# Kernel optimization log

Measured on AMD Instinct MI355X. Metric: run time of the kernel, lower is better.

Reference implementation:

```python
import jax, jax.numpy as jnp
import numpy as np

RADIUS = 8
STRIDE = 4
EPS = 1e-5
B, N, C, O = 4, 16384, 64, 64
S = 2 * RADIUS


def _bn(x, gamma, beta, mean, var):
    # inference-mode BatchNorm1d
    return (x - mean) / jnp.sqrt(var + EPS) * gamma + beta


def _circular_grouping_index(batch, n_points):
    # neighbors at circular offsets -radius..-1, 1..radius along the point sequence
    offsets = jnp.concatenate([jnp.arange(-RADIUS, 0), jnp.arange(1, RADIUS + 1)])  # (S,)
    idx = (jnp.arange(n_points)[:, None] + offsets[None, :]) % n_points             # (N,S)
    gidx = jnp.arange(batch)[:, None, None] * n_points + idx[None]                  # (B,N,S)
    return gidx.reshape(-1)


def setup_inputs() -> dict:
    key = jax.random.key(0)
    ks = jax.random.split(key, 8)
    inp = {
        "points": jax.random.normal(ks[0], (B, N, 2), dtype=jnp.float32),
        "features": jax.random.normal(ks[1], (B * N, C), dtype=jnp.float32),
        # modules_1: Linear(2+C -> C, no bias), BN(C), ReLU, Linear(C -> 1)
        "w1": jax.random.normal(ks[2], (2 + C, C), dtype=jnp.float32) * 0.05,
        "bn1_gamma": jnp.ones((C,), jnp.float32),
        "bn1_beta": jnp.zeros((C,), jnp.float32),
        "bn1_mean": jnp.zeros((C,), jnp.float32),
        "bn1_var": jnp.ones((C,), jnp.float32),
        "w2": jax.random.normal(ks[3], (C, 1), dtype=jnp.float32) * 0.05,
        "b2": jnp.zeros((1,), jnp.float32),
        # modules_2: Linear(C -> O, no bias), BN(O), ReLU
        "w3": jax.random.normal(ks[4], (C, O), dtype=jnp.float32) * 0.05,
        "bn2_gamma": jnp.ones((O,), jnp.float32),
        "bn2_beta": jnp.zeros((O,), jnp.float32),
        "bn2_mean": jnp.zeros((O,), jnp.float32),
        "bn2_var": jnp.ones((O,), jnp.float32),
    }
    return inp


def reference(points, features, w1, bn1_gamma, bn1_beta, bn1_mean, bn1_var,
              w2, b2, w3, bn2_gamma, bn2_beta, bn2_mean, bn2_var):
    batch, n_points, _ = points.shape
    gidx = _circular_grouping_index(batch, n_points)                 # (B*N*S,)

    nn_points = points.reshape(-1, 2)[gidx].reshape(batch, n_points, S, 2)
    translation = (nn_points - points[:, :, None])[:, ::STRIDE].reshape(-1, 2)

    nn_features = features[gidx].reshape(batch, n_points, S, -1)     # (B,N,S,C)
    nn_feat_str = nn_features[:, ::STRIDE].reshape(-1, features.shape[1])

    # attention weights
    h = jnp.concatenate([translation, nn_feat_str], axis=1) @ w1
    h = jax.nn.relu(_bn(h, bn1_gamma, bn1_beta, bn1_mean, bn1_var))
    w = h @ w2 + b2                                                  # (-1,1)
    w = jax.nn.softmax(w.reshape(-1, S, 1), axis=1)

    # value branch (computed on all gathered rows, then strided, as in original)
    y = jax.nn.relu(_bn(features[gidx] @ w3, bn2_gamma, bn2_beta, bn2_mean, bn2_var))
    y = y.reshape(batch, n_points, S, -1)[:, ::STRIDE].reshape(-1, S, O)

    outputs = jnp.sum(y * w, axis=1)                                 # (B*N/stride, O)
    points_out = points[:, ::STRIDE]
    return points_out, outputs
```

## Files before the change

kernel.cpp:

```cpp
#include <hip/hip_runtime.h>
#include <hip/hip_bf16.h>

#define NPTS   16384
#define NMASK  16383
#define EPSV   1e-5f
#define OUTOFF 32768

typedef __attribute__((ext_vector_type(8))) short short8_t;
typedef __attribute__((ext_vector_type(4))) short short4_t;
typedef __attribute__((ext_vector_type(4))) float f32x4;

static __device__ __forceinline__ short f2bf(float x) {
    union { __hip_bfloat16 b; short s; } u; u.b = __float2bfloat16(x); return u.s;
}
static __device__ __forceinline__ float bf2f(short s) {
    union { float f; unsigned u; } v; v.u = ((unsigned)(unsigned short)s) << 16; return v.f;
}

__global__ __launch_bounds__(512, 2) void fused_std_kernel(
    const float* __restrict__ points,
    const float* __restrict__ features,
    const float* __restrict__ w1,
    const float* __restrict__ bn1_gamma, const float* __restrict__ bn1_beta,
    const float* __restrict__ bn1_mean,  const float* __restrict__ bn1_var,
    const float* __restrict__ w2,
    const float* __restrict__ w3,
    const float* __restrict__ bn2_gamma, const float* __restrict__ bn2_beta,
    const float* __restrict__ bn2_mean,  const float* __restrict__ bn2_var,
    float* __restrict__ d_out)
{
    __shared__ __align__(16) short glds[288 * 64];
    __shared__ __align__(16) short ylds[288 * 64];
    __shared__ __align__(16) float ptsl[288 * 2];
    __shared__ __align__(16) float cst[448];
    __shared__ __align__(16) float ebuf[64][16];

    const float* cP  = cst;
    const float* cQ  = cst + 64;
    const float* cW2 = cst + 128;
    const float* cS1 = cst + 192;
    const float* cB1 = cst + 256;
    const float* cS2 = cst + 320;
    const float* cB2 = cst + 384;

    const int tid = threadIdx.x;
    const int wv  = tid >> 6, l = tid & 63;
    const int r   = l & 15,  kg = l >> 4;
    const int bi  = blockIdx.x >> 6;
    const int n0  = (blockIdx.x & 63) * 256;
    const int base = bi * NPTS;

    struct TF { float4 a, b, c, d; };
    auto loadTile = [&](int ti) {
        const int gr = base + ((n0 - 16 + ti * 16 + r) & NMASK);
        const float* fp = features + (size_t)gr * 64 + kg * 8;
        TF t;
        t.a = *(const float4*)(fp);
        t.b = *(const float4*)(fp + 4);
        t.c = *(const float4*)(fp + 32);
        t.d = *(const float4*)(fp + 36);
        return t;
    };
    TF Ta = loadTile(wv);
    TF Tb = loadTile(wv + 8);
    TF Tc;
    if (wv < 2) Tc = loadTile(16 + wv);

    short8_t wf[2][4][2];
    #pragma unroll
    for (int mat = 0; mat < 2; ++mat) {
        const float* wsrc = mat ? w3 : (w1 + 128);
        #pragma unroll
        for (int tt = 0; tt < 4; ++tt)
            #pragma unroll
            for (int s = 0; s < 2; ++s) {
                const float* p0 = wsrc + (s * 32 + kg * 8) * 64 + 16 * tt + r;
                short8_t w;
                #pragma unroll
                for (int e = 0; e < 8; ++e) w[e] = f2bf(p0[e * 64]);
                wf[mat][tt][s] = w;
            }
    }

    if (tid < 64) {
        const float s1 = bn1_gamma[tid] * rsqrtf(bn1_var[tid] + EPSV);
        cst[tid]       = s1 * w1[tid];
        cst[64 + tid]  = s1 * w1[64 + tid];
        cst[128 + tid] = w2[tid];
        cst[192 + tid] = s1;
        cst[256 + tid] = bn1_beta[tid] - bn1_mean[tid] * s1;
        const float s2 = bn2_gamma[tid] * rsqrtf(bn2_var[tid] + EPSV);
        cst[320 + tid] = s2;
        cst[384 + tid] = bn2_beta[tid] - bn2_mean[tid] * s2;
    }
    for (int t = tid; t < 288; t += 512) {
        const int gr = base + ((n0 - 16 + t) & NMASK);
        *(float2*)&ptsl[t * 2] = *(const float2*)&points[(size_t)gr * 2];
    }
    __syncthreads();

    auto mfma_tile = [&](const TF& t, int ti) {
        short8_t f0, f1;
        f0[0]=f2bf(t.a.x); f0[1]=f2bf(t.a.y); f0[2]=f2bf(t.a.z); f0[3]=f2bf(t.a.w);
        f0[4]=f2bf(t.b.x); f0[5]=f2bf(t.b.y); f0[6]=f2bf(t.b.z); f0[7]=f2bf(t.b.w);
        f1[0]=f2bf(t.c.x); f1[1]=f2bf(t.c.y); f1[2]=f2bf(t.c.z); f1[3]=f2bf(t.c.w);
        f1[4]=f2bf(t.d.x); f1[5]=f2bf(t.d.y); f1[6]=f2bf(t.d.z); f1[7]=f2bf(t.d.w);
        const f32x4 z = {0.f, 0.f, 0.f, 0.f};
        f32x4 acc0[4] = {z, z, z, z}, acc1[4] = {z, z, z, z};
        #pragma unroll
        for (int tt = 0; tt < 4; ++tt) {
            #pragma unroll
            for (int s = 0; s < 2; ++s) {
                acc0[tt] = __builtin_amdgcn_mfma_f32_16x16x32_bf16(wf[0][tt][s], s ? f1 : f0, acc0[tt], 0, 0, 0);
                acc1[tt] = __builtin_amdgcn_mfma_f32_16x16x32_bf16(wf[1][tt][s], s ? f1 : f0, acc1[tt], 0, 0, 0);
            }
        }
        const int row = ti * 16 + r;
        #pragma unroll
        for (int tt = 0; tt < 4; ++tt) {
            const int c0 = 16 * tt + kg * 4;
            short4_t gq, yq;
            #pragma unroll
            for (int j = 0; j < 4; ++j) {
                gq[j] = f2bf(fmaf(acc0[tt][j], cS1[c0 + j], cB1[c0 + j]));
                yq[j] = f2bf(fmaxf(fmaf(acc1[tt][j], cS2[c0 + j], cB2[c0 + j]), 0.0f));
            }
            const int byte = row * 128 +
                (((2 * tt + (kg >> 1)) ^ (row & 7)) << 4) + ((kg & 1) << 3);
            *(short4_t*)((char*)glds + byte) = gq;
            *(short4_t*)((char*)ylds + byte) = yq;
        }
    };
    mfma_tile(Ta, wv);
    mfma_tile(Tb, wv + 8);
    if (wv < 2) mfma_tile(Tc, 16 + wv);
    __syncthreads();

    const int offk = (r < 8) ? r - 8 : r - 7;
    const f32x4 P0a = *(const f32x4*)&cP[kg * 8],      P0b = *(const f32x4*)&cP[kg * 8 + 4];
    const f32x4 P1a = *(const f32x4*)&cP[32 + kg * 8], P1b = *(const f32x4*)&cP[32 + kg * 8 + 4];
    const f32x4 Q0a = *(const f32x4*)&cQ[kg * 8],      Q0b = *(const f32x4*)&cQ[kg * 8 + 4];
    const f32x4 Q1a = *(const f32x4*)&cQ[32 + kg * 8], Q1b = *(const f32x4*)&cQ[32 + kg * 8 + 4];
    const f32x4 Wa  = *(const f32x4*)&cW2[kg * 8],     Wb  = *(const f32x4*)&cW2[kg * 8 + 4];
    const f32x4 Wc  = *(const f32x4*)&cW2[32 + kg * 8],Wd  = *(const f32x4*)&cW2[32 + kg * 8 + 4];

    #pragma unroll 1
    for (int i = 0; i < 8; ++i) {
        const int p = wv * 8 + i;
        const int crow = 16 + 4 * p;
        const int nrow = crow + offk;
        const float2 cpt = *(const float2*)&ptsl[crow * 2];
        const float2 npt = *(const float2*)&ptsl[nrow * 2];
        const float tx = npt.x - cpt.x, ty = npt.y - cpt.y;
        const short8_t g0 = *(const short8_t*)((const char*)glds +
            nrow * 128 + ((kg ^ (nrow & 7)) << 4));
        const short8_t g1 = *(const short8_t*)((const char*)glds +
            nrow * 128 + (((4 + kg) ^ (nrow & 7)) << 4));
        float s = 0.0f;
        #pragma unroll
        for (int e = 0; e < 4; ++e) {
            s = fmaf(fmaxf(bf2f(g0[e])     + tx * P0a[e] + ty * Q0a[e], 0.f), Wa[e], s);
            s = fmaf(fmaxf(bf2f(g0[e + 4]) + tx * P0b[e] + ty * Q0b[e], 0.f), Wb[e], s);
            s = fmaf(fmaxf(bf2f(g1[e])     + tx * P1a[e] + ty * Q1a[e], 0.f), Wc[e], s);
            s = fmaf(fmaxf(bf2f(g1[e + 4]) + tx * P1b[e] + ty * Q1b[e], 0.f), Wd[e], s);
        }
        s += __shfl_xor(s, 16);
        s += __shfl_xor(s, 32);

        float mx = s;
        mx = fmaxf(mx, __shfl_xor(mx, 1));
        mx = fmaxf(mx, __shfl_xor(mx, 2));
        mx = fmaxf(mx, __shfl_xor(mx, 4));
        mx = fmaxf(mx, __shfl_xor(mx, 8));
        const float ex = __expf(s - mx);
        float se = ex;
        se += __shfl_xor(se, 1);
        se += __shfl_xor(se, 2);
        se += __shfl_xor(se, 4);
        se += __shfl_xor(se, 8);
        if (l < 16) ebuf[p][l] = ex / se;
    }
    asm volatile("s_waitcnt lgkmcnt(0)" ::: "memory");

    #pragma unroll 1
    for (int i = 0; i < 8; ++i) {
        const int p = wv * 8 + i;
        const int crow = 16 + 4 * p;
        const f32x4 wA = *(const f32x4*)&ebuf[p][0];
        const f32x4 wB = *(const f32x4*)&ebuf[p][4];
        const f32x4 wC = *(const f32x4*)&ebuf[p][8];
        const f32x4 wD = *(const f32x4*)&ebuf[p][12];
        float o = 0.0f;
        #pragma unroll
        for (int k = 0; k < 16; ++k) {
            const float wk = (k < 4) ? wA[k] : (k < 8) ? wB[k - 4]
                            : (k < 12) ? wC[k - 8] : wD[k - 12];
            const int rk = crow + ((k < 8) ? k - 8 : k - 7);
            const short yb = *(const short*)((const char*)ylds +
                rk * 128 + (((l >> 3) ^ (rk & 7)) << 4) + ((l & 7) << 1));
            o = fmaf(wk, bf2f(yb), o);
        }
        const int pl = ((blockIdx.x & 63) << 6) + p;
        d_out[OUTOFF + ((size_t)bi * 4096 + pl) * 64 + l] = o;
        if (l < 2)
            d_out[((size_t)bi * 4096 + pl) * 2 + l] = ptsl[crow * 2 + l];
    }
}

extern "C" void kernel_launch(void* const* d_in, const int* in_sizes, int n_in,
                              void* d_out, int out_size, void* d_ws, size_t ws_size,
                              hipStream_t stream)
{
    const float* points    = (const float*)d_in[0];
    const float* features  = (const float*)d_in[1];
    const float* w1        = (const float*)d_in[2];
    const float* bn1_gamma = (const float*)d_in[3];
    const float* bn1_beta  = (const float*)d_in[4];
    const float* bn1_mean  = (const float*)d_in[5];
    const float* bn1_var   = (const float*)d_in[6];
    const float* w2        = (const float*)d_in[7];
    const float* w3        = (const float*)d_in[9];
    const float* bn2_gamma = (const float*)d_in[10];
    const float* bn2_beta  = (const float*)d_in[11];
    const float* bn2_mean  = (const float*)d_in[12];
    const float* bn2_var   = (const float*)d_in[13];

    fused_std_kernel<<<256, 512, 0, stream>>>(
        points, features, w1, bn1_gamma, bn1_beta, bn1_mean, bn1_var,
        w2, w3, bn2_gamma, bn2_beta, bn2_mean, bn2_var, (float*)d_out);
}
```

Baseline: 20.75 us.

## Give each wave a private halo slice to drop the block-wide barrier

Each wave now computes the MFMA projections for its own 48-row window, which includes its halo, and stores them in a per-wave LDS slice. This replaces the shared 288-row buffer and the __syncthreads between the projection and attention phases with a per-wave lgkmcnt wait. In exchange, halo rows are recomputed, so every wave now does three tiles instead of two or three (48 rows per wave against 288 shared rows). LDS use also grows from 288 to 384 rows per buffer, which could limit occupancy.

```diff
diff --git a/kernel.cpp b/kernel.cpp
--- a/kernel.cpp
+++ b/kernel.cpp
@@ -29,8 +29,8 @@
     const float* __restrict__ bn2_mean,  const float* __restrict__ bn2_var,
     float* __restrict__ d_out)
 {
-    __shared__ __align__(16) short glds[288 * 64];
-    __shared__ __align__(16) short ylds[288 * 64];
+    __shared__ __align__(16) short glds[8][48 * 64];
+    __shared__ __align__(16) short ylds[8][48 * 64];
     __shared__ __align__(16) float ptsl[288 * 2];
     __shared__ __align__(16) float cst[448];
     __shared__ __align__(16) float ebuf[64][16];
@@ -49,10 +49,11 @@
     const int bi  = blockIdx.x >> 6;
     const int n0  = (blockIdx.x & 63) * 256;
     const int base = bi * NPTS;
+    const int Lw  = 32 * wv + 8;
 
     struct TF { float4 a, b, c, d; };
-    auto loadTile = [&](int ti) {
-        const int gr = base + ((n0 - 16 + ti * 16 + r) & NMASK);
+    auto loadTileL = [&](int lrow0) {
+        const int gr = base + ((n0 - 16 + lrow0 + r) & NMASK);
         const float* fp = features + (size_t)gr * 64 + kg * 8;
         TF t;
         t.a = *(const float4*)(fp);
@@ -61,10 +62,9 @@
         t.d = *(const float4*)(fp + 36);
         return t;
     };
-    TF Ta = loadTile(wv);
-    TF Tb = loadTile(wv + 8);
-    TF Tc;
-    if (wv < 2) Tc = loadTile(16 + wv);
+    TF Ta = loadTileL(Lw);
+    TF Tb = loadTileL(Lw + 16);
+    TF Tc = loadTileL(Lw + 32);
 
     short8_t wf[2][4][2];
     #pragma unroll
@@ -99,6 +99,8 @@
     }
     __syncthreads();
 
+    char* const gsl = (char*)glds[wv];
+    char* const ysl = (char*)ylds[wv];
     auto mfma_tile = [&](const TF& t, int ti) {
         short8_t f0, f1;
         f0[0]=f2bf(t.a.x); f0[1]=f2bf(t.a.y); f0[2]=f2bf(t.a.z); f0[3]=f2bf(t.a.w);
@@ -127,14 +129,14 @@
             }
             const int byte = row * 128 +
                 (((2 * tt + (kg >> 1)) ^ (row & 7)) << 4) + ((kg & 1) << 3);
-            *(short4_t*)((char*)glds + byte) = gq;
-            *(short4_t*)((char*)ylds + byte) = yq;
+            *(short4_t*)(gsl + byte) = gq;
+            *(short4_t*)(ysl + byte) = yq;
         }
     };
-    mfma_tile(Ta, wv);
-    mfma_tile(Tb, wv + 8);
-    if (wv < 2) mfma_tile(Tc, 16 + wv);
-    __syncthreads();
+    mfma_tile(Ta, 0);
+    mfma_tile(Tb, 1);
+    mfma_tile(Tc, 2);
+    asm volatile("s_waitcnt lgkmcnt(0)" ::: "memory");
 
     const int offk = (r < 8) ? r - 8 : r - 7;
     const f32x4 P0a = *(const f32x4*)&cP[kg * 8],      P0b = *(const f32x4*)&cP[kg * 8 + 4];
@@ -148,14 +150,15 @@
     for (int i = 0; i < 8; ++i) {
         const int p = wv * 8 + i;
         const int crow = 16 + 4 * p;
-        const int nrow = crow + offk;
+        const int cw   = 8 + 4 * i;
+        const int nw   = cw + offk;
         const float2 cpt = *(const float2*)&ptsl[crow * 2];
-        const float2 npt = *(const float2*)&ptsl[nrow * 2];
+        const float2 npt = *(const float2*)&ptsl[(crow + offk) * 2];
         const float tx = npt.x - cpt.x, ty = npt.y - cpt.y;
-        const short8_t g0 = *(const short8_t*)((const char*)glds +
-            nrow * 128 + ((kg ^ (nrow & 7)) << 4));
-        const short8_t g1 = *(const short8_t*)((const char*)glds +
-            nrow * 128 + (((4 + kg) ^ (nrow & 7)) << 4));
+        const short8_t g0 = *(const short8_t*)(gsl +
+            nw * 128 + ((kg ^ (nw & 7)) << 4));
+        const short8_t g1 = *(const short8_t*)(gsl +
+            nw * 128 + (((4 + kg) ^ (nw & 7)) << 4));
         float s = 0.0f;
         #pragma unroll
         for (int e = 0; e < 4; ++e) {
@@ -186,6 +189,7 @@
     for (int i = 0; i < 8; ++i) {
         const int p = wv * 8 + i;
         const int crow = 16 + 4 * p;
+        const int cw   = 8 + 4 * i;
         const f32x4 wA = *(const f32x4*)&ebuf[p][0];
         const f32x4 wB = *(const f32x4*)&ebuf[p][4];
         const f32x4 wC = *(const f32x4*)&ebuf[p][8];
@@ -195,8 +199,8 @@
         for (int k = 0; k < 16; ++k) {
             const float wk = (k < 4) ? wA[k] : (k < 8) ? wB[k - 4]
                             : (k < 12) ? wC[k - 8] : wD[k - 12];
-            const int rk = crow + ((k < 8) ? k - 8 : k - 7);
-            const short yb = *(const short*)((const char*)ylds +
+            const int rk = cw + ((k < 8) ? k - 8 : k - 7);
+            const short yb = *(const short*)(ysl +
                 rk * 128 + (((l >> 3) ^ (rk & 7)) << 4) + ((l & 7) << 1));
             o = fmaf(wk, bf2f(yb), o);
         }
```

New measurement: 21.20 us. 2.2% more time.
